# Kernel tuning notes

Measured on AMD Instinct MI355X. Metric: run time of the kernel, lower is better.

Reference implementation:

```python
import jax, jax.numpy as jnp
import numpy as np

B, N, IN_DIM, DIM, H, TOPK = 2, 2048, 256, 256, 8, 4
DH = DIM // H  # 32
EPS = 1e-5


def setup_inputs() -> dict:
    key = jax.random.key(0)
    ks = jax.random.split(key, 6)
    points = jax.random.normal(ks[0], (B * N, IN_DIM), dtype=jnp.float32)
    norm_gamma = jnp.ones((IN_DIM,), dtype=jnp.float32)
    norm_beta = jnp.zeros((IN_DIM,), dtype=jnp.float32)
    w_qkv = jax.random.normal(ks[1], (3 * DIM, IN_DIM), dtype=jnp.float32) / np.sqrt(IN_DIM)
    w_proj = jax.random.normal(ks[2], (DIM, DIM), dtype=jnp.float32) / np.sqrt(DIM)
    b_proj = jnp.zeros((DIM,), dtype=jnp.float32)
    return {"points": points, "norm_gamma": norm_gamma, "norm_beta": norm_beta,
            "w_qkv": w_qkv, "w_proj": w_proj, "b_proj": b_proj}


def reference(points, norm_gamma, norm_beta, w_qkv, w_proj, b_proj):
    # norm1 (LayerNorm over channel)
    x = points.reshape(B, N, IN_DIM)
    mu = jnp.mean(x, axis=-1, keepdims=True)
    var = jnp.var(x, axis=-1, keepdims=True)
    x = (x - mu) / jnp.sqrt(var + EPS) * norm_gamma + norm_beta
    # fused qkv: [B,N,3,H,DH]
    qkv = (x @ w_qkv.T).reshape(B, N, 3, H, DH)
    q, k, v = qkv[:, :, 0], qkv[:, :, 1], qkv[:, :, 2]  # [B,N,H,DH]
    # dense coarse attention: QK [B, M(query), S(key), H]
    qk = jnp.einsum('blhd,bshd->blsh', q, k)
    temp = 1.0 / np.sqrt(DH)
    A = jax.nn.softmax(temp * qk, axis=2)  # softmax over keys (dim=-2)
    # topk over key axis; zero out the top-k entries (scatter mask of zeros)
    A_t = jnp.transpose(A, (0, 1, 3, 2))  # [B,M,H,S]
    topk_score, topk_idx = jax.lax.top_k(A_t, TOPK)  # [B,M,H,k]
    bb = jnp.arange(B)[:, None, None, None]
    mm = jnp.arange(N)[None, :, None, None]
    hh = jnp.arange(H)[None, None, :, None]
    mask_t = jnp.ones_like(A_t).at[bb, mm, hh, topk_idx].set(0.0)
    # message = (A * mask) @ V
    message = jnp.einsum('blhs,bshd->blhd', A_t * mask_t, v).reshape(B, N, DIM)
    message = message @ w_proj.T + b_proj
    v_flat = v.reshape(B, N, DIM)
    message = v_flat + message
    # no padding (equal slens), so ~padding_mask selects everything -> flatten
    message_flat = message.reshape(B * N, DIM)
    topk_score_flat = jnp.transpose(topk_score, (0, 1, 3, 2)).reshape(B * N, TOPK, H)
    topk_idx_flat = jnp.transpose(topk_idx, (0, 1, 3, 2)).reshape(B * N, TOPK, H)
    return message_flat, topk_score_flat, topk_idx_flat
```

## Files before the change

### kernel.cpp

```cpp
#include <hip/hip_runtime.h>
#include <math.h>

#define B_ 2
#define N_ 2048
#define IN_DIM_ 256
#define DIM_ 256
#define H_ 8
#define DH_ 32
#define TOPK_ 4
#define EPS_ 1e-5f
#define TEMP_ 0.17677669529663687f
#define NT_ (N_ / 64)

__global__ __launch_bounds__(256) void ln_kernel(const float* __restrict__ x,
                                                 const float* __restrict__ gamma,
                                                 const float* __restrict__ beta,
                                                 float* __restrict__ xn) {
  int w = threadIdx.x >> 6, ld = threadIdx.x & 63;
  int row = blockIdx.x * 4 + w;
  const float4* xr = (const float4*)(x + (size_t)row * 256);
  float4 v = xr[ld];
  float s = v.x + v.y + v.z + v.w;
  float ss = v.x * v.x + v.y * v.y + v.z * v.z + v.w * v.w;
  #pragma unroll
  for (int off = 1; off < 64; off <<= 1) {
    s += __shfl_xor(s, off);
    ss += __shfl_xor(ss, off);
  }
  float mu = s * (1.0f / 256.0f);
  float var = ss * (1.0f / 256.0f) - mu * mu;
  float rstd = rsqrtf(var + EPS_);
  float4 g = ((const float4*)gamma)[ld];
  float4 bt = ((const float4*)beta)[ld];
  float4 o;
  o.x = (v.x - mu) * rstd * g.x + bt.x;
  o.y = (v.y - mu) * rstd * g.y + bt.y;
  o.z = (v.z - mu) * rstd * g.z + bt.z;
  o.w = (v.w - mu) * rstd * g.w + bt.w;
  ((float4*)(xn + (size_t)row * 256))[ld] = o;
}

template <bool PROJ>
__global__ __launch_bounds__(256) void gemm_nt(const float* __restrict__ A,
                                               const float* __restrict__ Bm,
                                               float* __restrict__ C,
                                               const float* __restrict__ vres,
                                               const float* __restrict__ bias,
                                               int K, int ldc) {
  __shared__ float As[32][64];
  __shared__ float Bs[32][64];
  int m0 = blockIdx.x * 64, n0 = blockIdx.y * 64;
  int t = threadIdx.x;
  int tm = t & 15, tn = t >> 4;
  float acc[4][4] = {};
  for (int k0 = 0; k0 < K; k0 += 32) {
    __syncthreads();
    for (int f = t; f < 512; f += 256) {
      int row = f >> 3, j = f & 7;
      float4 a = *(const float4*)(A + (size_t)(m0 + row) * K + k0 + j * 4);
      As[j * 4 + 0][row] = a.x; As[j * 4 + 1][row] = a.y;
      As[j * 4 + 2][row] = a.z; As[j * 4 + 3][row] = a.w;
      float4 b = *(const float4*)(Bm + (size_t)(n0 + row) * K + k0 + j * 4);
      Bs[j * 4 + 0][row] = b.x; Bs[j * 4 + 1][row] = b.y;
      Bs[j * 4 + 2][row] = b.z; Bs[j * 4 + 3][row] = b.w;
    }
    __syncthreads();
    #pragma unroll
    for (int k = 0; k < 32; k++) {
      float4 a = *(const float4*)&As[k][tm * 4];
      float4 b = *(const float4*)&Bs[k][tn * 4];
      float av[4] = {a.x, a.y, a.z, a.w};
      float bv[4] = {b.x, b.y, b.z, b.w};
      #pragma unroll
      for (int i = 0; i < 4; i++)
        #pragma unroll
        for (int j = 0; j < 4; j++)
          acc[i][j] = fmaf(av[i], bv[j], acc[i][j]);
    }
  }
  #pragma unroll
  for (int i = 0; i < 4; i++) {
    int m = m0 + tm * 4 + i;
    int n = n0 + tn * 4;
    float4 r = {acc[i][0], acc[i][1], acc[i][2], acc[i][3]};
    if (PROJ) {
      float4 vr = *(const float4*)(vres + (size_t)m * 768 + n);
      float4 bb = *(const float4*)(bias + n);
      r.x += vr.x + bb.x; r.y += vr.y + bb.y;
      r.z += vr.z + bb.z; r.w += vr.w + bb.w;
    }
    *(float4*)(C + (size_t)m * ldc + n) = r;
  }
}


__device__ __forceinline__ void stage16(const float* g, float* l) {
  __builtin_amdgcn_global_load_lds(
      (const __attribute__((address_space(1))) unsigned int*)g,
      (__attribute__((address_space(3))) unsigned int*)l, 16, 0, 0);
}

__global__ __launch_bounds__(512, 2) void attn_kernel(const float* __restrict__ qkv,
                                                      float* __restrict__ msg,
                                                      float* __restrict__ out_s,
                                                      float* __restrict__ out_i) {
  const int lin = blockIdx.x;
  const int logical = (lin & 7) * 128 + (lin >> 3);
  const int bh = logical >> 6;
  const int rt = logical & 63;
  const int b = bh >> 3, h = bh & 7;
  const int l0 = rt * 32;

  const int t = threadIdx.x;
  const int wid = __builtin_amdgcn_readfirstlane(t >> 6);
  const int lane = t & 63;
  const int r = lane & 31;
  const int hf16 = (lane >> 5) << 4;
  const int c0 = wid * 8;

  __shared__ float Ks[2][2048];
  __shared__ float Vs[2][2048];
  __shared__ float Pl[8][32];
  __shared__ float Ptv[8][32][5];
  __shared__ int   Pti[8][32][5];
  __shared__ float AccO[32][33];
  __shared__ float Fsc[32][4];
  __shared__ int   Ffi[32][4];
  __shared__ float Flinv[32];

  const float* qrow = qkv + ((size_t)(b * N_) + l0 + r) * 768 + h * DH_ + hf16;
  float4 q[4];
  #pragma unroll
  for (int j = 0; j < 4; j++) {
    float4 v = ((const float4*)qrow)[j];
    v.x *= TEMP_; v.y *= TEMP_; v.z *= TEMP_; v.w *= TEMP_;
    q[j] = v;
  }

  float4 o[4];
  #pragma unroll
  for (int j = 0; j < 4; j++) o[j] = make_float4(0.f, 0.f, 0.f, 0.f);
  float l = 0.f;
  float tv[4];
  int ti[4];
  #pragma unroll
  for (int i = 0; i < 4; i++) { tv[i] = -INFINITY; ti[i] = 0x7fffffff; }

  const int scol = t >> 3, sch = t & 7;
  const float* gK0 = qkv + (size_t)(b * N_) * 768 + 256 + h * DH_ +
                     (size_t)scol * 768 + sch * 4;
  float* lK = &Ks[0][0] + wid * 256;
  float* lV = &Vs[0][0] + wid * 256;

#define STAGE(bb, s0)                                          \
  do {                                                         \
    const float* gk_ = gK0 + (size_t)(s0) * 768;               \
    stage16(gk_, lK + (bb) * 2048);                            \
    stage16(gk_ + 256, lV + (bb) * 2048);                      \
  } while (0)

  STAGE(0, 0);
  asm volatile("s_waitcnt vmcnt(0)" ::: "memory");
  __syncthreads();

  #pragma unroll 1
  for (int t0 = 0; t0 < NT_; ++t0) {
    const int cur = t0 & 1;
    const int s0 = t0 * 64;
    if (t0 + 1 < NT_) STAGE(cur ^ 1, s0 + 64);

    const float* Kc = Ks[cur];
    const float* Vc = Vs[cur];

    #pragma unroll
    for (int c = 0; c < 8; ++c) {
      const int cc = c0 + c;
      const int gc = s0 + cc;

      const float4* kp = (const float4*)&Kc[cc * 32 + hf16];
      float4 a = make_float4(0.f, 0.f, 0.f, 0.f);
      #pragma unroll
      for (int j = 0; j < 4; ++j) {
        float4 kv = kp[j];
        a.x = fmaf(q[j].x, kv.x, a.x);
        a.y = fmaf(q[j].y, kv.y, a.y);
        a.z = fmaf(q[j].z, kv.z, a.z);
        a.w = fmaf(q[j].w, kv.w, a.w);
      }
      float svh = (a.x + a.y) + (a.z + a.w);
      float sv = svh + __shfl_xor(svh, 32);

      if (sv > tv[3] || (sv == tv[3] && gc < ti[3])) {
        bool i2 = (sv > tv[2]) || (sv == tv[2] && gc < ti[2]);
        bool i1 = (sv > tv[1]) || (sv == tv[1] && gc < ti[1]);
        bool i0 = (sv > tv[0]) || (sv == tv[0] && gc < ti[0]);
        tv[3] = i2 ? tv[2] : sv; ti[3] = i2 ? ti[2] : gc;
        float nv2 = i1 ? tv[1] : sv; int ni2 = i1 ? ti[1] : gc;
        float nv1 = i0 ? tv[0] : sv; int ni1 = i0 ? ti[0] : gc;
        if (i2) { tv[2] = nv2; ti[2] = ni2; }
        if (i1) { tv[1] = nv1; ti[1] = ni1; }
        if (i0) { tv[0] = sv; ti[0] = gc; }
      }

      float p = __expf(sv);
      l += p;
      const float4* vp = (const float4*)&Vc[cc * 32 + hf16];
      #pragma unroll
      for (int j = 0; j < 4; ++j) {
        float4 vv = vp[j];
        o[j].x = fmaf(p, vv.x, o[j].x);
        o[j].y = fmaf(p, vv.y, o[j].y);
        o[j].z = fmaf(p, vv.z, o[j].z);
        o[j].w = fmaf(p, vv.w, o[j].w);
      }
    }

    asm volatile("s_waitcnt vmcnt(0)" ::: "memory");
    __syncthreads();
  }
#undef STAGE

  if (lane < 32) {
    Pl[wid][r] = l;
    #pragma unroll
    for (int i = 0; i < 4; ++i) { Ptv[wid][r][i] = tv[i]; Pti[wid][r][i] = ti[i]; }
  }
  for (int i = t; i < 32 * 33; i += 512) (&AccO[0][0])[i] = 0.f;
  __syncthreads();

  #pragma unroll
  for (int j = 0; j < 4; ++j) {
    atomicAdd(&AccO[r][hf16 + j * 4 + 0], o[j].x);
    atomicAdd(&AccO[r][hf16 + j * 4 + 1], o[j].y);
    atomicAdd(&AccO[r][hf16 + j * 4 + 2], o[j].z);
    atomicAdd(&AccO[r][hf16 + j * 4 + 3], o[j].w);
  }
  __syncthreads();

  if (wid == 0 && lane < 32) {
    float lg = 0.f;
    #pragma unroll
    for (int j = 0; j < 8; ++j) lg += Pl[j][r];
    float linv = 1.f / lg;
    Flinv[r] = linv;
    float fv[4];
    int fi[4];
    #pragma unroll
    for (int rr = 0; rr < 4; ++rr) {
      float best = -INFINITY;
      int bi = 0x7fffffff, bj = 0, bii = 0;
      #pragma unroll
      for (int j = 0; j < 8; ++j)
        #pragma unroll
        for (int i2 = 0; i2 < 4; ++i2) {
          float v2 = Ptv[j][r][i2];
          int ix = Pti[j][r][i2];
          if (v2 > best || (v2 == best && ix < bi)) { best = v2; bi = ix; bj = j; bii = i2; }
        }
      Ptv[bj][r][bii] = -INFINITY;
      fv[rr] = best;
      fi[rr] = bi;
    }
    size_t base = ((size_t)(b * N_) + l0 + r) * TOPK_;
    #pragma unroll
    for (int rr = 0; rr < 4; ++rr) {
      float sc = __expf(fv[rr]) * linv;
      Fsc[r][rr] = sc;
      Ffi[r][rr] = fi[rr];
      out_s[(base + rr) * H_ + h] = sc;
      out_i[(base + rr) * H_ + h] = (float)fi[rr];
    }
  }
  __syncthreads();

  if (t < 256) {
    int rr = t >> 3, dc = t & 7;
    float linv = Flinv[rr];
    float ax = AccO[rr][dc * 4 + 0] * linv;
    float ay = AccO[rr][dc * 4 + 1] * linv;
    float az = AccO[rr][dc * 4 + 2] * linv;
    float aw2 = AccO[rr][dc * 4 + 3] * linv;
    #pragma unroll
    for (int k = 0; k < 4; ++k) {
      int idx = Ffi[rr][k];
      float sc = Fsc[rr][k];
      const float* vp = qkv + ((size_t)(b * N_) + idx) * 768 + 512 + h * DH_ + dc * 4;
      float4 vv = *(const float4*)vp;
      ax = fmaf(-sc, vv.x, ax); ay = fmaf(-sc, vv.y, ay);
      az = fmaf(-sc, vv.z, az); aw2 = fmaf(-sc, vv.w, aw2);
    }
    float4 r4 = {ax, ay, az, aw2};
    *(float4*)(msg + ((size_t)(b * N_) + l0 + rr) * DIM_ + h * DH_ + dc * 4) = r4;
  }
}

extern "C" void kernel_launch(void* const* d_in, const int* in_sizes, int n_in,
                              void* d_out, int out_size, void* d_ws, size_t ws_size,
                              hipStream_t stream) {
  const float* points = (const float*)d_in[0];
  const float* norm_gamma = (const float*)d_in[1];
  const float* norm_beta = (const float*)d_in[2];
  const float* w_qkv = (const float*)d_in[3];
  const float* w_proj = (const float*)d_in[4];
  const float* b_proj = (const float*)d_in[5];

  float* out0 = (float*)d_out;
  float* out1 = out0 + (size_t)4096 * 256;
  float* out2 = out1 + (size_t)4096 * 4 * 8;

  float* xn = (float*)d_ws;
  float* qkv = xn + (size_t)4096 * 256;
  float* msg = qkv + (size_t)4096 * 768;

  ln_kernel<<<1024, 256, 0, stream>>>(points, norm_gamma, norm_beta, xn);
  gemm_nt<false><<<dim3(64, 12), 256, 0, stream>>>(xn, w_qkv, qkv, nullptr,
                                                   nullptr, 256, 768);
  attn_kernel<<<1024, 512, 0, stream>>>(qkv, msg, out1, out2);
  gemm_nt<true><<<dim3(64, 4), 256, 0, stream>>>(msg, w_proj, out0, qkv + 512,
                                                 b_proj, 256, 256);
}
```

Before: 539.7 us.

## Process two query rows per lane to double K/V reuse in attention

Each attention block now handles 64 query rows instead of 32, with every lane holding two query vectors and two sets of accumulators and top-k state. Each K/V tile staged into LDS is reused for twice as many queries, which halves global K/V traffic and the number of LDS reads per FMA. In exchange, register pressure rises, grid size halves to 512 blocks (which may reduce occupancy and latency hiding), and the per-query serial work per lane doubles.

```diff
diff --git a/kernel.cpp b/kernel.cpp
--- a/kernel.cpp
+++ b/kernel.cpp
@@ -105,11 +105,11 @@
                                                       float* __restrict__ out_s,
                                                       float* __restrict__ out_i) {
   const int lin = blockIdx.x;
-  const int logical = (lin & 7) * 128 + (lin >> 3);
-  const int bh = logical >> 6;
-  const int rt = logical & 63;
+  const int logical = (lin & 7) * 64 + (lin >> 3);
+  const int bh = logical >> 5;
+  const int rt = logical & 31;
   const int b = bh >> 3, h = bh & 7;
-  const int l0 = rt * 32;
+  const int l0 = rt * 64;
 
   const int t = threadIdx.x;
   const int wid = __builtin_amdgcn_readfirstlane(t >> 6);
@@ -120,31 +120,40 @@
 
   __shared__ float Ks[2][2048];
   __shared__ float Vs[2][2048];
-  __shared__ float Pl[8][32];
-  __shared__ float Ptv[8][32][5];
-  __shared__ int   Pti[8][32][5];
-  __shared__ float AccO[32][33];
-  __shared__ float Fsc[32][4];
-  __shared__ int   Ffi[32][4];
-  __shared__ float Flinv[32];
-
-  const float* qrow = qkv + ((size_t)(b * N_) + l0 + r) * 768 + h * DH_ + hf16;
-  float4 q[4];
+  __shared__ float Pl[8][64];
+  __shared__ float Ptv[8][64][5];
+  __shared__ int   Pti[8][64][5];
+  __shared__ float AccO[64][33];
+  __shared__ float Fsc[64][4];
+  __shared__ int   Ffi[64][4];
+  __shared__ float Flinv[64];
+
+  const float* qr0 = qkv + ((size_t)(b * N_) + l0 + r) * 768 + h * DH_ + hf16;
+  float4 q0[4], q1[4];
   #pragma unroll
   for (int j = 0; j < 4; j++) {
-    float4 v = ((const float4*)qrow)[j];
+    float4 v = ((const float4*)qr0)[j];
     v.x *= TEMP_; v.y *= TEMP_; v.z *= TEMP_; v.w *= TEMP_;
-    q[j] = v;
-  }
-
-  float4 o[4];
-  #pragma unroll
-  for (int j = 0; j < 4; j++) o[j] = make_float4(0.f, 0.f, 0.f, 0.f);
-  float l = 0.f;
-  float tv[4];
-  int ti[4];
-  #pragma unroll
-  for (int i = 0; i < 4; i++) { tv[i] = -INFINITY; ti[i] = 0x7fffffff; }
+    q0[j] = v;
+    float4 w = *(const float4*)(qr0 + 32 * 768 + j * 4);
+    w.x *= TEMP_; w.y *= TEMP_; w.z *= TEMP_; w.w *= TEMP_;
+    q1[j] = w;
+  }
+
+  float4 o0[4], o1[4];
+  #pragma unroll
+  for (int j = 0; j < 4; j++) {
+    o0[j] = make_float4(0.f, 0.f, 0.f, 0.f);
+    o1[j] = make_float4(0.f, 0.f, 0.f, 0.f);
+  }
+  float la = 0.f, lb = 0.f;
+  float tv0[4], tv1[4];
+  int ti0[4], ti1[4];
+  #pragma unroll
+  for (int i = 0; i < 4; i++) {
+    tv0[i] = -INFINITY; ti0[i] = 0x7fffffff;
+    tv1[i] = -INFINITY; ti1[i] = 0x7fffffff;
+  }
 
   const int scol = t >> 3, sch = t & 7;
   const float* gK0 = qkv + (size_t)(b * N_) * 768 + 256 + h * DH_ +
@@ -178,40 +187,64 @@
       const int gc = s0 + cc;
 
       const float4* kp = (const float4*)&Kc[cc * 32 + hf16];
-      float4 a = make_float4(0.f, 0.f, 0.f, 0.f);
+      float4 a0 = make_float4(0.f, 0.f, 0.f, 0.f);
+      float4 a1 = make_float4(0.f, 0.f, 0.f, 0.f);
       #pragma unroll
       for (int j = 0; j < 4; ++j) {
         float4 kv = kp[j];
-        a.x = fmaf(q[j].x, kv.x, a.x);
-        a.y = fmaf(q[j].y, kv.y, a.y);
-        a.z = fmaf(q[j].z, kv.z, a.z);
-        a.w = fmaf(q[j].w, kv.w, a.w);
+        a0.x = fmaf(q0[j].x, kv.x, a0.x);
+        a0.y = fmaf(q0[j].y, kv.y, a0.y);
+        a0.z = fmaf(q0[j].z, kv.z, a0.z);
+        a0.w = fmaf(q0[j].w, kv.w, a0.w);
+        a1.x = fmaf(q1[j].x, kv.x, a1.x);
+        a1.y = fmaf(q1[j].y, kv.y, a1.y);
+        a1.z = fmaf(q1[j].z, kv.z, a1.z);
+        a1.w = fmaf(q1[j].w, kv.w, a1.w);
       }
-      float svh = (a.x + a.y) + (a.z + a.w);
-      float sv = svh + __shfl_xor(svh, 32);
-
-      if (sv > tv[3] || (sv == tv[3] && gc < ti[3])) {
-        bool i2 = (sv > tv[2]) || (sv == tv[2] && gc < ti[2]);
-        bool i1 = (sv > tv[1]) || (sv == tv[1] && gc < ti[1]);
-        bool i0 = (sv > tv[0]) || (sv == tv[0] && gc < ti[0]);
-        tv[3] = i2 ? tv[2] : sv; ti[3] = i2 ? ti[2] : gc;
-        float nv2 = i1 ? tv[1] : sv; int ni2 = i1 ? ti[1] : gc;
-        float nv1 = i0 ? tv[0] : sv; int ni1 = i0 ? ti[0] : gc;
-        if (i2) { tv[2] = nv2; ti[2] = ni2; }
-        if (i1) { tv[1] = nv1; ti[1] = ni1; }
-        if (i0) { tv[0] = sv; ti[0] = gc; }
+      float sh0 = (a0.x + a0.y) + (a0.z + a0.w);
+      float sh1 = (a1.x + a1.y) + (a1.z + a1.w);
+      float sv0 = sh0 + __shfl_xor(sh0, 32);
+      float sv1 = sh1 + __shfl_xor(sh1, 32);
+
+      if (sv0 > tv0[3] || (sv0 == tv0[3] && gc < ti0[3])) {
+        bool i2 = (sv0 > tv0[2]) || (sv0 == tv0[2] && gc < ti0[2]);
+        bool i1 = (sv0 > tv0[1]) || (sv0 == tv0[1] && gc < ti0[1]);
+        bool i0 = (sv0 > tv0[0]) || (sv0 == tv0[0] && gc < ti0[0]);
+        tv0[3] = i2 ? tv0[2] : sv0; ti0[3] = i2 ? ti0[2] : gc;
+        float nv2 = i1 ? tv0[1] : sv0; int ni2 = i1 ? ti0[1] : gc;
+        float nv1 = i0 ? tv0[0] : sv0; int ni1 = i0 ? ti0[0] : gc;
+        if (i2) { tv0[2] = nv2; ti0[2] = ni2; }
+        if (i1) { tv0[1] = nv1; ti0[1] = ni1; }
+        if (i0) { tv0[0] = sv0; ti0[0] = gc; }
       }
-
-      float p = __expf(sv);
-      l += p;
+      if (sv1 > tv1[3] || (sv1 == tv1[3] && gc < ti1[3])) {
+        bool i2 = (sv1 > tv1[2]) || (sv1 == tv1[2] && gc < ti1[2]);
+        bool i1 = (sv1 > tv1[1]) || (sv1 == tv1[1] && gc < ti1[1]);
+        bool i0 = (sv1 > tv1[0]) || (sv1 == tv1[0] && gc < ti1[0]);
+        tv1[3] = i2 ? tv1[2] : sv1; ti1[3] = i2 ? ti1[2] : gc;
+        float nv2 = i1 ? tv1[1] : sv1; int ni2 = i1 ? ti1[1] : gc;
+        float nv1 = i0 ? tv1[0] : sv1; int ni1 = i0 ? ti1[0] : gc;
+        if (i2) { tv1[2] = nv2; ti1[2] = ni2; }
+        if (i1) { tv1[1] = nv1; ti1[1] = ni1; }
+        if (i0) { tv1[0] = sv1; ti1[0] = gc; }
+      }
+
+      float p0 = __expf(sv0);
+      float p1 = __expf(sv1);
+      la += p0;
+      lb += p1;
       const float4* vp = (const float4*)&Vc[cc * 32 + hf16];
       #pragma unroll
       for (int j = 0; j < 4; ++j) {
         float4 vv = vp[j];
-        o[j].x = fmaf(p, vv.x, o[j].x);
-        o[j].y = fmaf(p, vv.y, o[j].y);
-        o[j].z = fmaf(p, vv.z, o[j].z);
-        o[j].w = fmaf(p, vv.w, o[j].w);
+        o0[j].x = fmaf(p0, vv.x, o0[j].x);
+        o0[j].y = fmaf(p0, vv.y, o0[j].y);
+        o0[j].z = fmaf(p0, vv.z, o0[j].z);
+        o0[j].w = fmaf(p0, vv.w, o0[j].w);
+        o1[j].x = fmaf(p1, vv.x, o1[j].x);
+        o1[j].y = fmaf(p1, vv.y, o1[j].y);
+        o1[j].z = fmaf(p1, vv.z, o1[j].z);
+        o1[j].w = fmaf(p1, vv.w, o1[j].w);
       }
     }
 
@@ -221,28 +254,37 @@
 #undef STAGE
 
   if (lane < 32) {
-    Pl[wid][r] = l;
-    #pragma unroll
-    for (int i = 0; i < 4; ++i) { Ptv[wid][r][i] = tv[i]; Pti[wid][r][i] = ti[i]; }
-  }
-  for (int i = t; i < 32 * 33; i += 512) (&AccO[0][0])[i] = 0.f;
+    Pl[wid][r] = la;
+    Pl[wid][r + 32] = lb;
+    #pragma unroll
+    for (int i = 0; i < 4; ++i) {
+      Ptv[wid][r][i] = tv0[i]; Pti[wid][r][i] = ti0[i];
+      Ptv[wid][r + 32][i] = tv1[i]; Pti[wid][r + 32][i] = ti1[i];
+    }
+  }
+  for (int i = t; i < 64 * 33; i += 512) (&AccO[0][0])[i] = 0.f;
   __syncthreads();
 
   #pragma unroll
   for (int j = 0; j < 4; ++j) {
-    atomicAdd(&AccO[r][hf16 + j * 4 + 0], o[j].x);
-    atomicAdd(&AccO[r][hf16 + j * 4 + 1], o[j].y);
-    atomicAdd(&AccO[r][hf16 + j * 4 + 2], o[j].z);
-    atomicAdd(&AccO[r][hf16 + j * 4 + 3], o[j].w);
+    atomicAdd(&AccO[r][hf16 + j * 4 + 0], o0[j].x);
+    atomicAdd(&AccO[r][hf16 + j * 4 + 1], o0[j].y);
+    atomicAdd(&AccO[r][hf16 + j * 4 + 2], o0[j].z);
+    atomicAdd(&AccO[r][hf16 + j * 4 + 3], o0[j].w);
+    atomicAdd(&AccO[r + 32][hf16 + j * 4 + 0], o1[j].x);
+    atomicAdd(&AccO[r + 32][hf16 + j * 4 + 1], o1[j].y);
+    atomicAdd(&AccO[r + 32][hf16 + j * 4 + 2], o1[j].z);
+    atomicAdd(&AccO[r + 32][hf16 + j * 4 + 3], o1[j].w);
   }
   __syncthreads();
 
-  if (wid == 0 && lane < 32) {
+  if (wid < 2 && lane < 32) {
+    const int row = wid * 32 + r;
     float lg = 0.f;
     #pragma unroll
-    for (int j = 0; j < 8; ++j) lg += Pl[j][r];
+    for (int j = 0; j < 8; ++j) lg += Pl[j][row];
     float linv = 1.f / lg;
-    Flinv[r] = linv;
+    Flinv[row] = linv;
     float fv[4];
     int fi[4];
     #pragma unroll
@@ -253,27 +295,27 @@
       for (int j = 0; j < 8; ++j)
         #pragma unroll
         for (int i2 = 0; i2 < 4; ++i2) {
-          float v2 = Ptv[j][r][i2];
-          int ix = Pti[j][r][i2];
+          float v2 = Ptv[j][row][i2];
+          int ix = Pti[j][row][i2];
           if (v2 > best || (v2 == best && ix < bi)) { best = v2; bi = ix; bj = j; bii = i2; }
         }
-      Ptv[bj][r][bii] = -INFINITY;
+      Ptv[bj][row][bii] = -INFINITY;
       fv[rr] = best;
       fi[rr] = bi;
     }
-    size_t base = ((size_t)(b * N_) + l0 + r) * TOPK_;
+    size_t base = ((size_t)(b * N_) + l0 + row) * TOPK_;
     #pragma unroll
     for (int rr = 0; rr < 4; ++rr) {
       float sc = __expf(fv[rr]) * linv;
-      Fsc[r][rr] = sc;
-      Ffi[r][rr] = fi[rr];
+      Fsc[row][rr] = sc;
+      Ffi[row][rr] = fi[rr];
       out_s[(base + rr) * H_ + h] = sc;
       out_i[(base + rr) * H_ + h] = (float)fi[rr];
     }
   }
   __syncthreads();
 
-  if (t < 256) {
+  {
     int rr = t >> 3, dc = t & 7;
     float linv = Flinv[rr];
     float ax = AccO[rr][dc * 4 + 0] * linv;
@@ -315,7 +357,7 @@
   ln_kernel<<<1024, 256, 0, stream>>>(points, norm_gamma, norm_beta, xn);
   gemm_nt<false><<<dim3(64, 12), 256, 0, stream>>>(xn, w_qkv, qkv, nullptr,
                                                    nullptr, 256, 768);
-  attn_kernel<<<1024, 512, 0, stream>>>(qkv, msg, out1, out2);
+  attn_kernel<<<512, 512, 0, stream>>>(qkv, msg, out1, out2);
   gemm_nt<true><<<dim3(64, 4), 256, 0, stream>>>(msg, w_proj, out0, qkv + 512,
                                                  b_proj, 256, 256);
 }
```

Measured after the change: 456.9 us. 1.18x faster.
